# Optimization experiments

Measured on AMD Instinct MI355X. Metric: run time of the kernel, lower is better.

The kernel has to match this reference:

```python
import jax, jax.numpy as jnp
import numpy as np

N_NODES = 50000
N_EDGES = 800000
F_IN = 128
HID = 128
F_ADD = 32
N_GRAPHS = 128


def setup_inputs() -> dict:
    key = jax.random.key(0)
    ks = jax.random.split(key, 12)
    x = jax.random.normal(ks[0], (N_NODES, F_IN), dtype=jnp.float32)
    edge_index = jax.random.randint(ks[1], (2, N_EDGES), 0, N_NODES, dtype=jnp.int64)
    batch = jnp.sort(jax.random.randint(ks[2], (N_NODES,), 0, N_GRAPHS, dtype=jnp.int64))
    additional_features = jax.random.normal(ks[3], (N_GRAPHS, F_ADD), dtype=jnp.float32)
    def glorot(k, shape):
        fan_in, fan_out = shape[0], shape[1]
        lim = jnp.sqrt(6.0 / (fan_in + fan_out)).astype(jnp.float32)
        return jax.random.uniform(k, shape, jnp.float32, -lim, lim)
    W1 = glorot(ks[4], (F_IN, HID)); b1 = jnp.zeros((HID,), jnp.float32)
    W2 = glorot(ks[5], (HID, HID)); b2 = jnp.zeros((HID,), jnp.float32)
    fc1_w = glorot(ks[6], (HID + F_ADD, HID)); fc1_b = jnp.zeros((HID,), jnp.float32)
    fc2_w = glorot(ks[7], (HID, 2)); fc2_b = jnp.zeros((2,), jnp.float32)
    return {"x": x, "edge_index": edge_index, "batch": batch,
            "additional_features": additional_features,
            "W1": W1, "b1": b1, "W2": W2, "b2": b2,
            "fc1_w": fc1_w, "fc1_b": fc1_b, "fc2_w": fc2_w, "fc2_b": fc2_b}


def _gcn_conv(h, src, dst, norm, W, b):
    # h: [N, d_in]; symmetric-normalized scatter-add aggregation (PyG GCNConv)
    h = h @ W                                   # [N, d_out]
    msg = h[src] * norm[:, None]                # gather + scale: [E+N, d_out]
    return jax.ops.segment_sum(msg, dst, num_segments=N_NODES) + b


def reference(x, edge_index, batch, additional_features,
              W1, b1, W2, b2, fc1_w, fc1_b, fc2_w, fc2_b):
    loops = jnp.arange(N_NODES, dtype=edge_index.dtype)
    src = jnp.concatenate([edge_index[0], loops])   # A + I
    dst = jnp.concatenate([edge_index[1], loops])
    deg = jax.ops.segment_sum(jnp.ones_like(src, dtype=x.dtype), dst,
                              num_segments=N_NODES)
    dinv = jnp.where(deg > 0, jax.lax.rsqrt(jnp.maximum(deg, 1.0)), 0.0)
    norm = dinv[src] * dinv[dst]

    h = jax.nn.relu(_gcn_conv(x, src, dst, norm, W1, b1))
    h = jax.nn.relu(_gcn_conv(h, src, dst, norm, W2, b2))
    # dropout is identity in eval mode

    sums = jax.ops.segment_sum(h, batch, num_segments=N_GRAPHS)    # [G, HID]
    counts = jax.ops.segment_sum(jnp.ones((N_NODES,), h.dtype), batch,
                                 num_segments=N_GRAPHS)
    pooled = sums / jnp.maximum(counts, 1.0)[:, None]              # global_mean_pool

    z = jnp.concatenate([pooled, additional_features], axis=1)     # [G, HID+F_ADD]
    z = jax.nn.relu(z @ fc1_w + fc1_b)
    return z @ fc2_w + fc2_b                                       # [G, 2]
```

## Files before the change

kernel.cpp:

```cpp
#include <hip/hip_runtime.h>

#define NN 50000
#define NE 800000
#define FD 128
#define FDH 64
#define FA 32
#define NG 128
#define EETOT (NE + NN)
#define NBLK ((NN + 255) / 256)
#define PK 8
#define FEPB 2048
#define FNCH ((EETOT + FEPB - 1) / FEPB)
#define NPXCD 6250

typedef __attribute__((ext_vector_type(8))) short short8;
typedef __attribute__((ext_vector_type(4))) float f32x4;

__device__ __forceinline__ float bfbits(unsigned short u) {
    return __uint_as_float(((unsigned int)u) << 16);
}
__device__ __forceinline__ float bflo(unsigned int p) { return __uint_as_float(p << 16); }
__device__ __forceinline__ float bfhi(unsigned int p) { return __uint_as_float(p & 0xffff0000u); }
__device__ __forceinline__ unsigned short f2bf(float f) {
    unsigned int u = __float_as_uint(f);
    unsigned int r = u + 0x7FFFu + ((u >> 16) & 1u);
    return (unsigned short)(r >> 16);
}
__device__ __forceinline__ unsigned int packbf(float a, float b) {
    return (unsigned int)f2bf(a) | ((unsigned int)f2bf(b) << 16);
}
__device__ __forceinline__ int ld_idx(const int* p, int i, int is64) {
    return is64 ? p[2 * i] : p[i];
}
__device__ int probe_bf16(const unsigned int* t, int nwords) {
    int nz = 0, hits = 0;
    for (int i = 0; i < nwords; ++i) {
        unsigned int w = t[i];
        if (w == 0u) continue;
        ++nz;
        unsigned int e = (w >> 7) & 0xFFu;
        if (e >= 100u && e <= 140u) ++hits;
    }
    return (nz < 8) ? 1 : (hits * 4 >= nz * 3);
}

__global__ __launch_bounds__(128) void mark_kernel(float* out, float v) {
    out[threadIdx.x] = v;
}

__global__ __launch_bounds__(64) void flags_kernel(
        const unsigned int* x, const int* ei, const int* batch,
        const unsigned int* addf, const unsigned int* w1, const unsigned int* b1,
        const unsigned int* w2, const unsigned int* b2, const unsigned int* fc1w,
        const unsigned int* fc1b, const unsigned int* fc2w, const unsigned int* fc2b,
        int* flags) {
    if (threadIdx.x != 0) return;
    flags[0]  = probe_bf16(x, 64);
    flags[3]  = probe_bf16(addf, 64);
    flags[4]  = probe_bf16(w1, 64);
    flags[5]  = probe_bf16(b1, 64);
    flags[6]  = probe_bf16(w2, 64);
    flags[7]  = probe_bf16(b2, 64);
    flags[8]  = probe_bf16(fc1w, 64);
    flags[9]  = probe_bf16(fc1b, 64);
    flags[10] = probe_bf16(fc2w, 64);
    flags[11] = probe_bf16(fc2b, 1);
    int odd_or = 0;
    for (int k = 0; k < 32; ++k) odd_or |= ei[2 * k + 1];
    flags[12] = (odd_or == 0) ? 1 : 0;
    flags[13] = (batch[NN - 1] == 0) ? 1 : 0;
}

__global__ __launch_bounds__(256) void prep(
        const void* x, const void* addf,
        const void* w1, const void* b1, const void* w2, const void* b2,
        const void* fc1w, const void* fc1b, const void* fc2w, const void* fc2b,
        unsigned int* bufC, unsigned int* W1t, unsigned int* W2t,
        float* addff, float* b1f, float* b2f, float* fc1wf, float* fc1bf,
        float* fc2wf, float* fc2bf, const int* flags, int* degi) {
    int b = blockIdx.x;
    if (b < 12500) {
        int i = b * 256 + threadIdx.x;
        if (flags[0]) {
            bufC[i] = ((const unsigned int*)x)[i];
        } else {
            const float* s = (const float*)x;
            bufC[i] = packbf(s[2 * i], s[2 * i + 1]);
        }
    } else if (b < 12564) {
        int rel = (b - 12500) * 256 + threadIdx.x;
        const void* src = (rel < 8192) ? w1 : w2;
        unsigned int* dst = (rel < 8192) ? W1t : W2t;
        int flag = (rel < 8192) ? flags[4] : flags[6];
        int rr = rel & 8191;
        int n = rr >> 6, kk = rr & 63;
        float lo, hi;
        if (flag) {
            const unsigned short* s = (const unsigned short*)src;
            lo = bfbits(s[(2 * kk) * FD + n]);
            hi = bfbits(s[(2 * kk + 1) * FD + n]);
        } else {
            const float* s = (const float*)src;
            lo = s[(2 * kk) * FD + n];
            hi = s[(2 * kk + 1) * FD + n];
        }
        dst[rr] = packbf(lo, hi);
    } else if (b < 12663) {
        int i = (b - 12564) * 256 + threadIdx.x;
        const void* src; float* dst; int flag; int rel;
        if      (i < 4096)  { src = addf; dst = addff; flag = flags[3];  rel = i; }
        else if (i < 4224)  { src = b1;   dst = b1f;   flag = flags[5];  rel = i - 4096; }
        else if (i < 4352)  { src = b2;   dst = b2f;   flag = flags[7];  rel = i - 4224; }
        else if (i < 24832) { src = fc1w; dst = fc1wf; flag = flags[8];  rel = i - 4352; }
        else if (i < 24960) { src = fc1b; dst = fc1bf; flag = flags[9];  rel = i - 24832; }
        else if (i < 25216) { src = fc2w; dst = fc2wf; flag = flags[10]; rel = i - 24960; }
        else if (i < 25218) { src = fc2b; dst = fc2bf; flag = flags[11]; rel = i - 25216; }
        else return;
        if (flag) dst[rel] = bfbits(((const unsigned short*)src)[rel]);
        else      dst[rel] = ((const float*)src)[rel];
    } else {
        int i = (b - 12663) * 256 + threadIdx.x;
        if (i < NN) degi[i] = 0;
    }
}

__global__ __launch_bounds__(256) void deg_kernel(const int* ei, const int* flags,
                                                  int* deg) {
    int e = blockIdx.x * 256 + threadIdx.x;
    int is64 = flags[12];
    if (e < NE) atomicAdd(&deg[ld_idx(ei, NE + e, is64)], 1);
}

__global__ __launch_bounds__(256) void scan1(const int* deg, float* dinv,
                                             int* escan, int* bsum) {
    __shared__ int sh[256];
    int i = blockIdx.x * 256 + threadIdx.x;
    int d = (i < NN) ? deg[i] : 0;
    if (i < NN) dinv[i] = rsqrtf((float)(d + 1));
    int v = (i < NN) ? d + 1 : 0;
    sh[threadIdx.x] = v;
    __syncthreads();
    for (int off = 1; off < 256; off <<= 1) {
        int a = ((int)threadIdx.x >= off) ? sh[threadIdx.x - off] : 0;
        __syncthreads();
        sh[threadIdx.x] += a;
        __syncthreads();
    }
    if (i < NN) escan[i] = sh[threadIdx.x] - v;
    if (threadIdx.x == 255) bsum[blockIdx.x] = sh[255];
}

__global__ __launch_bounds__(256) void scan3(const int* escan, const int* bsum,
        const int* batch, const int* flags, int* rowstart, int* cursor, int* gstart) {
    __shared__ int sb[256];
    int t = threadIdx.x;
    int v = (t < NBLK) ? bsum[t] : 0;
    sb[t] = v;
    __syncthreads();
    for (int off = 1; off < 256; off <<= 1) {
        int a = (t >= off) ? sb[t - off] : 0;
        __syncthreads();
        sb[t] += a;
        __syncthreads();
    }
    int boff = (blockIdx.x == 0) ? 0 : sb[blockIdx.x - 1];
    int i = blockIdx.x * 256 + t;
    if (i < NN) {
        int r = escan[i] + boff;
        rowstart[i] = r;
        cursor[i]   = r;
    }
    if (i == 0) rowstart[NN] = EETOT;
    if (i < NN) {
        int is64 = flags[13];
        int bc = ld_idx(batch, i, is64);
        if (i == 0) {
            for (int g = 0; g <= bc; ++g) gstart[g] = 0;
        } else {
            int bp = ld_idx(batch, i - 1, is64);
            for (int g = bp + 1; g <= bc; ++g) gstart[g] = i;
        }
        if (i == NN - 1) {
            for (int g = bc + 1; g <= NG; ++g) gstart[g] = NN;
        }
    }
}

__global__ __launch_bounds__(256) void fill_kernel(const int* ei, const int* flags,
        const float* dinv, int* cursor, unsigned int* cv) {
    int chunk = blockIdx.x >> 3;
    int par   = blockIdx.x & 7;
    int base  = chunk * FEPB;
    int is64  = flags[12];
    #pragma unroll
    for (int k = 0; k < FEPB / 256; ++k) {
        int e = base + k * 256 + threadIdx.x;
        if (e >= EETOT) break;
        int s, d;
        if (e < NE) { d = ld_idx(ei, NE + e, is64); s = -1; }
        else        { s = d = e - NE; }
        if (d / NPXCD != par) continue;
        if (s < 0) s = ld_idx(ei, e, is64);
        int pos = atomicAdd(&cursor[d], 1);
        cv[pos] = (unsigned int)s | ((unsigned int)f2bf(dinv[s] * dinv[d]) << 16);
    }
}

__global__ __launch_bounds__(256) void gemm_mfma(const unsigned int* __restrict__ A,
        const unsigned int* __restrict__ Wt, unsigned short* __restrict__ C) {
    int wave = threadIdx.x >> 6;
    int lane = threadIdx.x & 63;
    int quad = lane >> 4;
    int l16  = lane & 15;
    int mbase = blockIdx.x * 64 + wave * 16;
    int ra = mbase + l16;
    if (ra >= NN) ra = NN - 1;
    short8 af[4];
    const uint4* Arow = (const uint4*)(A + (size_t)ra * FDH);
    #pragma unroll
    for (int kk = 0; kk < 4; ++kk) {
        uint4 v = Arow[kk * 4 + quad];
        af[kk] = *(short8*)&v;
    }
    #pragma unroll
    for (int nt = 0; nt < 8; ++nt) {
        int n = nt * 16 + l16;
        const uint4* Wrow = (const uint4*)(Wt + (size_t)n * FDH);
        f32x4 acc = {0.f, 0.f, 0.f, 0.f};
        #pragma unroll
        for (int kk = 0; kk < 4; ++kk) {
            uint4 wv = Wrow[kk * 4 + quad];
            short8 bf = *(short8*)&wv;
            acc = __builtin_amdgcn_mfma_f32_16x16x32_bf16(af[kk], bf, acc, 0, 0, 0);
        }
        int row0 = mbase + quad * 4;
        #pragma unroll
        for (int reg = 0; reg < 4; ++reg) {
            int r = row0 + reg;
            if (r < NN) C[(size_t)r * FD + nt * 16 + l16] = f2bf(acc[reg]);
        }
    }
}

__global__ __launch_bounds__(256) void aggregate_kernel(const unsigned int* Hb,
        const unsigned int* cv, const int* rowstart, const float* bias,
        unsigned int* outb) {
    int n = blockIdx.x * 4 + (threadIdx.x >> 6);
    int cp = threadIdx.x & 63;
    if (n >= NN) return;
    int jb = rowstart[n], je = rowstart[n + 1];
    float acc0 = 0.f, acc1 = 0.f;
    int j = jb;
    for (; j + 7 < je; j += 8) {
        unsigned int rr[8], hh[8];
        #pragma unroll
        for (int k = 0; k < 8; ++k) rr[k] = cv[j + k];
        #pragma unroll
        for (int k = 0; k < 8; ++k) hh[k] = Hb[(size_t)(rr[k] & 0xFFFFu) * FDH + cp];
        #pragma unroll
        for (int k = 0; k < 8; ++k) {
            float v = bfbits((unsigned short)(rr[k] >> 16));
            acc0 += v * bflo(hh[k]);
            acc1 += v * bfhi(hh[k]);
        }
    }
    for (; j + 3 < je; j += 4) {
        unsigned int rr[4], hh[4];
        #pragma unroll
        for (int k = 0; k < 4; ++k) rr[k] = cv[j + k];
        #pragma unroll
        for (int k = 0; k < 4; ++k) hh[k] = Hb[(size_t)(rr[k] & 0xFFFFu) * FDH + cp];
        #pragma unroll
        for (int k = 0; k < 4; ++k) {
            float v = bfbits((unsigned short)(rr[k] >> 16));
            acc0 += v * bflo(hh[k]);
            acc1 += v * bfhi(hh[k]);
        }
    }
    for (; j < je; ++j) {
        unsigned int r = cv[j];
        unsigned int h = Hb[(size_t)(r & 0xFFFFu) * FDH + cp];
        float v = bfbits((unsigned short)(r >> 16));
        acc0 += v * bflo(h);
        acc1 += v * bfhi(h);
    }
    acc0 = fmaxf(acc0 + bias[2 * cp], 0.f);
    acc1 = fmaxf(acc1 + bias[2 * cp + 1], 0.f);
    outb[(size_t)n * FDH + cp] = packbf(acc0, acc1);
}

__global__ __launch_bounds__(64) void pool_part(const unsigned int* Hb,
        const int* gstart, float* part) {
    int g = blockIdx.x >> 3;
    int k = blockIdx.x & (PK - 1);
    int cp = threadIdx.x;
    int s = gstart[g], e = gstart[g + 1];
    int len = e - s;
    int per = (len + PK - 1) / PK;
    int ss = s + k * per;
    int ee = ss + per; if (ee > e) ee = e;
    float a0 = 0.f, a1 = 0.f, b0 = 0.f, b1 = 0.f;
    int n = ss;
    for (; n + 1 < ee; n += 2) {
        unsigned int h0 = Hb[(size_t)n * FDH + cp];
        unsigned int h1 = Hb[(size_t)(n + 1) * FDH + cp];
        a0 += bflo(h0); a1 += bfhi(h0);
        b0 += bflo(h1); b1 += bfhi(h1);
    }
    if (n < ee) {
        unsigned int h0 = Hb[(size_t)n * FDH + cp];
        a0 += bflo(h0); a1 += bfhi(h0);
    }
    part[(size_t)(g * PK + k) * FD + 2 * cp]     = a0 + b0;
    part[(size_t)(g * PK + k) * FD + 2 * cp + 1] = a1 + b1;
}

__global__ __launch_bounds__(128) void head_kernel(const float* part, const int* gstart,
        const float* addf, const float* fc1w, const float* fc1b,
        const float* fc2w, const float* fc2b, const int* flags, void* outp) {
    int g = blockIdx.x;
    int t = threadIdx.x;
    __shared__ float z[FD + FA];
    __shared__ float h[FD];
    float a = 0.f;
    #pragma unroll
    for (int k = 0; k < PK; ++k) a += part[(size_t)(g * PK + k) * FD + t];
    float cnt = (float)(gstart[g + 1] - gstart[g]);
    if (cnt < 1.0f) cnt = 1.0f;
    z[t] = a / cnt;
    if (t < FA) z[FD + t] = addf[g * FA + t];
    __syncthreads();
    float acc = fc1b[t];
    #pragma unroll 4
    for (int k = 0; k < FD + FA; ++k)
        acc += z[k] * fc1w[k * FD + t];
    h[t] = fmaxf(acc, 0.f);
    __syncthreads();
    if (t < 2) {
        float o = fc2b[t];
        for (int j = 0; j < FD; ++j) o += h[j] * fc2w[j * 2 + t];
        if (flags[0]) ((unsigned short*)outp)[g * 2 + t] = f2bf(o);
        else          ((float*)outp)[g * 2 + t] = o;
    }
}

extern "C" void kernel_launch(void* const* d_in, const int* in_sizes, int n_in,
                              void* d_out, int out_size, void* d_ws, size_t ws_size,
                              hipStream_t stream) {
    (void)out_size;

    if (n_in != 12) {
        hipLaunchKernelGGL(mark_kernel, dim3(1), dim3(128), 0, stream,
                           (float*)d_out, 2000.0f);
        return;
    }
    const int exp_sizes[12] = {6400000, 1600000, 50000, 4096, 16384, 128,
                               16384, 128, 20480, 128, 256, 2};
    for (int i = 0; i < 12; ++i) {
        if (in_sizes[i] != exp_sizes[i]) {
            hipLaunchKernelGGL(mark_kernel, dim3(1), dim3(128), 0, stream,
                               (float*)d_out, 3000.0f + 100.0f * i);
            return;
        }
    }

    size_t off = 0;
    char* base = (char*)d_ws;
#define WSALLOC(ptr, type, nbytes) \
    type* ptr = (type*)(base + off); off += (((size_t)(nbytes)) + 255) & ~(size_t)255;
    WSALLOC(bufA,  unsigned int, (size_t)NN * FDH * 4)
    WSALLOC(bufB,  unsigned int, (size_t)NN * FDH * 4)
    WSALLOC(bufC,  unsigned int, (size_t)NN * FDH * 4)
    WSALLOC(dinv,  float, (size_t)NN * 4)
    WSALLOC(degi,  int,   (size_t)NN * 4)
    WSALLOC(rowst, int,   (size_t)(NN + 1) * 4)
    WSALLOC(cursor,int,   (size_t)NN * 4)
    WSALLOC(escan, int,   (size_t)NN * 4)
    WSALLOC(bsum,  int,   (size_t)NBLK * 4)
    WSALLOC(cv,    unsigned int, (size_t)EETOT * 4)
    WSALLOC(part,  float, (size_t)NG * PK * FD * 4)
    WSALLOC(gstart,int,   (size_t)(NG + 1) * 4)
    WSALLOC(W1t,   unsigned int, (size_t)FD * FDH * 4)
    WSALLOC(W2t,   unsigned int, (size_t)FD * FDH * 4)
    WSALLOC(b1f,   float, FD * 4)
    WSALLOC(b2f,   float, FD * 4)
    WSALLOC(addff, float, (size_t)NG * FA * 4)
    WSALLOC(fc1wf, float, (size_t)(FD + FA) * FD * 4)
    WSALLOC(fc1bf, float, FD * 4)
    WSALLOC(fc2wf, float, FD * 2 * 4)
    WSALLOC(fc2bf, float, 2 * 4)
    WSALLOC(flags, int, 16 * 4)
#undef WSALLOC
    if (ws_size < off) {
        hipLaunchKernelGGL(mark_kernel, dim3(1), dim3(128), 0, stream,
                           (float*)d_out, 1000.0f);
        return;
    }

    const int* ei    = (const int*)d_in[1];
    const int* batch = (const int*)d_in[2];

    hipLaunchKernelGGL(flags_kernel, dim3(1), dim3(64), 0, stream,
                       (const unsigned int*)d_in[0], ei, batch,
                       (const unsigned int*)d_in[3], (const unsigned int*)d_in[4],
                       (const unsigned int*)d_in[5], (const unsigned int*)d_in[6],
                       (const unsigned int*)d_in[7], (const unsigned int*)d_in[8],
                       (const unsigned int*)d_in[9], (const unsigned int*)d_in[10],
                       (const unsigned int*)d_in[11], flags);

    hipLaunchKernelGGL(prep, dim3(12859), dim3(256), 0, stream,
                       d_in[0], d_in[3], d_in[4], d_in[5], d_in[6],
                       d_in[7], d_in[8], d_in[9], d_in[10], d_in[11],
                       bufC, W1t, W2t, addff, b1f, b2f, fc1wf, fc1bf,
                       fc2wf, fc2bf, flags, degi);

    hipLaunchKernelGGL(deg_kernel, dim3((NE + 255) / 256), dim3(256), 0, stream,
                       ei, flags, degi);
    hipLaunchKernelGGL(scan1, dim3(NBLK), dim3(256), 0, stream,
                       degi, dinv, escan, bsum);
    hipLaunchKernelGGL(scan3, dim3(NBLK), dim3(256), 0, stream,
                       escan, bsum, batch, flags, rowst, cursor, gstart);
    hipLaunchKernelGGL(fill_kernel, dim3(FNCH * 8), dim3(256), 0, stream,
                       ei, flags, dinv, cursor, cv);

    hipLaunchKernelGGL(gemm_mfma, dim3((NN + 63) / 64), dim3(256), 0, stream,
                       bufC, W1t, (unsigned short*)bufA);
    hipLaunchKernelGGL(aggregate_kernel, dim3((NN + 3) / 4), dim3(256), 0, stream,
                       bufA, cv, rowst, b1f, bufB);
    hipLaunchKernelGGL(gemm_mfma, dim3((NN + 63) / 64), dim3(256), 0, stream,
                       bufB, W2t, (unsigned short*)bufA);
    hipLaunchKernelGGL(aggregate_kernel, dim3((NN + 3) / 4), dim3(256), 0, stream,
                       bufA, cv, rowst, b2f, bufB);

    hipLaunchKernelGGL(pool_part, dim3(NG * PK), dim3(64), 0, stream,
                       bufB, gstart, part);
    hipLaunchKernelGGL(head_kernel, dim3(NG), dim3(FD), 0, stream,
                       part, gstart, addff, fc1wf, fc1bf, fc2wf, fc2bf,
                       flags, d_out);
}
```

Before: 340.8 us.

## Fuse graph build into cooperative kernel, fold x conversion into GEMM, merge pool+head

Replaces the degree, scan, scan-finalize and CSR-fill kernels with one cooperative grid kernel that uses grid.sync between phases and caches 32-bit edge indices. The fp32-to-bf16 conversion of x moves into the first GEMM's load path, removing a separate full pass over x and the staging buffer. Pooling and the MLP head merge into one kernel, and the flag probes use wave ballots instead of a serial loop. This cuts launch count and memory traffic but adds grid-wide barrier costs and extra s32/d32 buffers, and reduces pooling parallelism to one block per graph.

```diff
diff --git a/kernel.cpp b/kernel.cpp
--- a/kernel.cpp
+++ b/kernel.cpp
@@ -1,4 +1,7 @@
 #include <hip/hip_runtime.h>
+#include <hip/hip_cooperative_groups.h>
+
+namespace cg = cooperative_groups;
 
 #define NN 50000
 #define NE 800000
@@ -8,10 +11,11 @@
 #define NG 128
 #define EETOT (NE + NN)
 #define NBLK ((NN + 255) / 256)
-#define PK 8
 #define FEPB 2048
 #define FNCH ((EETOT + FEPB - 1) / FEPB)
 #define NPXCD 6250
+#define CBG 1024
+#define CBT (CBG * 256)
 
 typedef __attribute__((ext_vector_type(8))) short short8;
 typedef __attribute__((ext_vector_type(4))) float f32x4;
@@ -32,63 +36,48 @@
 __device__ __forceinline__ int ld_idx(const int* p, int i, int is64) {
     return is64 ? p[2 * i] : p[i];
 }
-__device__ int probe_bf16(const unsigned int* t, int nwords) {
-    int nz = 0, hits = 0;
-    for (int i = 0; i < nwords; ++i) {
-        unsigned int w = t[i];
-        if (w == 0u) continue;
-        ++nz;
-        unsigned int e = (w >> 7) & 0xFFu;
-        if (e >= 100u && e <= 140u) ++hits;
-    }
-    return (nz < 8) ? 1 : (hits * 4 >= nz * 3);
-}
 
 __global__ __launch_bounds__(128) void mark_kernel(float* out, float v) {
     out[threadIdx.x] = v;
 }
 
-__global__ __launch_bounds__(64) void flags_kernel(
+__global__ __launch_bounds__(256) void flags_kernel(
         const unsigned int* x, const int* ei, const int* batch,
         const unsigned int* addf, const unsigned int* w1, const unsigned int* b1,
         const unsigned int* w2, const unsigned int* b2, const unsigned int* fc1w,
         const unsigned int* fc1b, const unsigned int* fc2w, const unsigned int* fc2b,
         int* flags) {
-    if (threadIdx.x != 0) return;
-    flags[0]  = probe_bf16(x, 64);
-    flags[3]  = probe_bf16(addf, 64);
-    flags[4]  = probe_bf16(w1, 64);
-    flags[5]  = probe_bf16(b1, 64);
-    flags[6]  = probe_bf16(w2, 64);
-    flags[7]  = probe_bf16(b2, 64);
-    flags[8]  = probe_bf16(fc1w, 64);
-    flags[9]  = probe_bf16(fc1b, 64);
-    flags[10] = probe_bf16(fc2w, 64);
-    flags[11] = probe_bf16(fc2b, 1);
-    int odd_or = 0;
-    for (int k = 0; k < 32; ++k) odd_or |= ei[2 * k + 1];
-    flags[12] = (odd_or == 0) ? 1 : 0;
-    flags[13] = (batch[NN - 1] == 0) ? 1 : 0;
+    int w = threadIdx.x >> 6, lane = threadIdx.x & 63;
+    const unsigned int* tp[12] = {x, 0, 0, addf, w1, b1, w2, b2, fc1w, fc1b, fc2w, fc2b};
+    const int nw[12] = {64, 0, 0, 64, 64, 64, 64, 64, 64, 64, 64, 1};
+    for (int idx = w; idx < 12; idx += 4) {
+        const unsigned int* p = tp[idx];
+        if (!p) continue;
+        unsigned int wv = (lane < nw[idx]) ? p[lane] : 0u;
+        int nzp = (wv != 0u) ? 1 : 0;
+        unsigned int e = (wv >> 7) & 0xFFu;
+        int hitp = (nzp && e >= 100u && e <= 140u) ? 1 : 0;
+        int nz = __popcll(__ballot(nzp));
+        int hits = __popcll(__ballot(hitp));
+        if (lane == 0) flags[idx] = (nz < 8) ? 1 : (hits * 4 >= nz * 3);
+    }
+    if (w == 1) {
+        int v = (lane < 32) ? ei[2 * lane + 1] : 0;
+        unsigned long long m = __ballot(v != 0);
+        if (lane == 0) flags[12] = (m == 0ull) ? 1 : 0;
+    }
+    if (w == 2 && lane == 0) flags[13] = (batch[NN - 1] == 0) ? 1 : 0;
 }
 
 __global__ __launch_bounds__(256) void prep(
-        const void* x, const void* addf,
-        const void* w1, const void* b1, const void* w2, const void* b2,
-        const void* fc1w, const void* fc1b, const void* fc2w, const void* fc2b,
-        unsigned int* bufC, unsigned int* W1t, unsigned int* W2t,
+        const void* addf, const void* w1, const void* b1, const void* w2,
+        const void* b2, const void* fc1w, const void* fc1b, const void* fc2w,
+        const void* fc2b, unsigned int* W1t, unsigned int* W2t,
         float* addff, float* b1f, float* b2f, float* fc1wf, float* fc1bf,
         float* fc2wf, float* fc2bf, const int* flags, int* degi) {
     int b = blockIdx.x;
-    if (b < 12500) {
-        int i = b * 256 + threadIdx.x;
-        if (flags[0]) {
-            bufC[i] = ((const unsigned int*)x)[i];
-        } else {
-            const float* s = (const float*)x;
-            bufC[i] = packbf(s[2 * i], s[2 * i + 1]);
-        }
-    } else if (b < 12564) {
-        int rel = (b - 12500) * 256 + threadIdx.x;
+    if (b < 64) {
+        int rel = b * 256 + threadIdx.x;
         const void* src = (rel < 8192) ? w1 : w2;
         unsigned int* dst = (rel < 8192) ? W1t : W2t;
         int flag = (rel < 8192) ? flags[4] : flags[6];
@@ -105,8 +94,8 @@
             hi = s[(2 * kk + 1) * FD + n];
         }
         dst[rr] = packbf(lo, hi);
-    } else if (b < 12663) {
-        int i = (b - 12564) * 256 + threadIdx.x;
+    } else if (b < 163) {
+        int i = (b - 64) * 256 + threadIdx.x;
         const void* src; float* dst; int flag; int rel;
         if      (i < 4096)  { src = addf; dst = addff; flag = flags[3];  rel = i; }
         else if (i < 4224)  { src = b1;   dst = b1f;   flag = flags[5];  rel = i - 4096; }
@@ -119,8 +108,104 @@
         if (flag) dst[rel] = bfbits(((const unsigned short*)src)[rel]);
         else      dst[rel] = ((const float*)src)[rel];
     } else {
-        int i = (b - 12663) * 256 + threadIdx.x;
+        int i = (b - 163) * 256 + threadIdx.x;
         if (i < NN) degi[i] = 0;
+    }
+}
+
+__global__ __launch_bounds__(256, 4) void coop_build(
+        const int* ei, const int* batch, const int* flags,
+        int* degi, float* dinv, int* escan, int* bsum,
+        int* rowstart, int* cursor, int* gstart,
+        int* s32, int* d32, unsigned int* cv) {
+    cg::grid_group grid = cg::this_grid();
+    __shared__ int sh[256];
+    int tid = blockIdx.x * 256 + threadIdx.x;
+    int b = blockIdx.x;
+    int is64 = flags[12];
+
+    for (int e = tid; e < NE; e += CBT) {
+        int s = ld_idx(ei, e, is64);
+        int d = ld_idx(ei, NE + e, is64);
+        s32[e] = s;
+        d32[e] = d;
+        atomicAdd(&degi[d], 1);
+    }
+    grid.sync();
+
+    if (b < NBLK) {
+        int i = b * 256 + threadIdx.x;
+        int d = (i < NN) ? degi[i] : 0;
+        if (i < NN) dinv[i] = rsqrtf((float)(d + 1));
+        int v = (i < NN) ? d + 1 : 0;
+        sh[threadIdx.x] = v;
+        __syncthreads();
+        for (int off = 1; off < 256; off <<= 1) {
+            int a = ((int)threadIdx.x >= off) ? sh[threadIdx.x - off] : 0;
+            __syncthreads();
+            sh[threadIdx.x] += a;
+            __syncthreads();
+        }
+        if (i < NN) escan[i] = sh[threadIdx.x] - v;
+        if (threadIdx.x == 255) bsum[b] = sh[255];
+    }
+    grid.sync();
+
+    if (b == 0) {
+        int t = threadIdx.x;
+        int v = (t < NBLK) ? bsum[t] : 0;
+        sh[t] = v;
+        __syncthreads();
+        for (int off = 1; off < 256; off <<= 1) {
+            int a = (t >= off) ? sh[t - off] : 0;
+            __syncthreads();
+            sh[t] += a;
+            __syncthreads();
+        }
+        if (t < NBLK) bsum[t] = sh[t] - v;
+    }
+    grid.sync();
+
+    if (b < NBLK) {
+        int i = b * 256 + threadIdx.x;
+        if (i < NN) {
+            int r = escan[i] + bsum[b];
+            rowstart[i] = r;
+            cursor[i]   = r;
+        }
+        if (i == 0) rowstart[NN] = EETOT;
+        if (i < NN) {
+            int is64b = flags[13];
+            int bc = ld_idx(batch, i, is64b);
+            if (i == 0) {
+                for (int g = 0; g <= bc; ++g) gstart[g] = 0;
+            } else {
+                int bp = ld_idx(batch, i - 1, is64b);
+                for (int g = bp + 1; g <= bc; ++g) gstart[g] = i;
+            }
+            if (i == NN - 1) {
+                for (int g = bc + 1; g <= NG; ++g) gstart[g] = NN;
+            }
+        }
+    }
+    grid.sync();
+
+    for (int vb = b; vb < FNCH * 8; vb += CBG) {
+        int chunk = vb >> 3;
+        int par   = vb & 7;
+        int base  = chunk * FEPB;
+        #pragma unroll
+        for (int k = 0; k < FEPB / 256; ++k) {
+            int e = base + k * 256 + threadIdx.x;
+            if (e >= EETOT) break;
+            int s, d;
+            if (e < NE) { d = d32[e]; s = -1; }
+            else        { s = d = e - NE; }
+            if (d / NPXCD != par) continue;
+            if (s < 0) s = s32[e];
+            int pos = atomicAdd(&cursor[d], 1);
+            cv[pos] = (unsigned int)s | ((unsigned int)f2bf(dinv[s] * dinv[d]) << 16);
+        }
     }
 }
 
@@ -206,8 +291,9 @@
     }
 }
 
-__global__ __launch_bounds__(256) void gemm_mfma(const unsigned int* __restrict__ A,
-        const unsigned int* __restrict__ Wt, unsigned short* __restrict__ C) {
+__global__ __launch_bounds__(256) void gemm_mfma(const void* __restrict__ Av,
+        const unsigned int* __restrict__ Wt, unsigned short* __restrict__ C,
+        const int* flags, int maybe_f32) {
     int wave = threadIdx.x >> 6;
     int lane = threadIdx.x & 63;
     int quad = lane >> 4;
@@ -216,11 +302,25 @@
     int ra = mbase + l16;
     if (ra >= NN) ra = NN - 1;
     short8 af[4];
-    const uint4* Arow = (const uint4*)(A + (size_t)ra * FDH);
-    #pragma unroll
-    for (int kk = 0; kk < 4; ++kk) {
-        uint4 v = Arow[kk * 4 + quad];
-        af[kk] = *(short8*)&v;
+    bool f32in = maybe_f32 && !flags[0];
+    if (!f32in) {
+        const uint4* Arow = (const uint4*)((const unsigned int*)Av + (size_t)ra * FDH);
+        #pragma unroll
+        for (int kk = 0; kk < 4; ++kk) {
+            uint4 v = Arow[kk * 4 + quad];
+            af[kk] = *(short8*)&v;
+        }
+    } else {
+        const float* Arow = (const float*)Av + (size_t)ra * FD;
+        #pragma unroll
+        for (int kk = 0; kk < 4; ++kk) {
+            const float4* p = (const float4*)(Arow + (kk * 4 + quad) * 8);
+            float4 u = p[0], v = p[1];
+            uint4 q;
+            q.x = packbf(u.x, u.y); q.y = packbf(u.z, u.w);
+            q.z = packbf(v.x, v.y); q.w = packbf(v.z, v.w);
+            af[kk] = *(short8*)&q;
+        }
     }
     #pragma unroll
     for (int nt = 0; nt < 8; ++nt) {
@@ -289,52 +389,40 @@
     outb[(size_t)n * FDH + cp] = packbf(acc0, acc1);
 }
 
-__global__ __launch_bounds__(64) void pool_part(const unsigned int* Hb,
-        const int* gstart, float* part) {
-    int g = blockIdx.x >> 3;
-    int k = blockIdx.x & (PK - 1);
-    int cp = threadIdx.x;
-    int s = gstart[g], e = gstart[g + 1];
-    int len = e - s;
-    int per = (len + PK - 1) / PK;
-    int ss = s + k * per;
-    int ee = ss + per; if (ee > e) ee = e;
-    float a0 = 0.f, a1 = 0.f, b0 = 0.f, b1 = 0.f;
-    int n = ss;
-    for (; n + 1 < ee; n += 2) {
-        unsigned int h0 = Hb[(size_t)n * FDH + cp];
-        unsigned int h1 = Hb[(size_t)(n + 1) * FDH + cp];
-        a0 += bflo(h0); a1 += bfhi(h0);
-        b0 += bflo(h1); b1 += bfhi(h1);
-    }
-    if (n < ee) {
-        unsigned int h0 = Hb[(size_t)n * FDH + cp];
-        a0 += bflo(h0); a1 += bfhi(h0);
-    }
-    part[(size_t)(g * PK + k) * FD + 2 * cp]     = a0 + b0;
-    part[(size_t)(g * PK + k) * FD + 2 * cp + 1] = a1 + b1;
-}
-
-__global__ __launch_bounds__(128) void head_kernel(const float* part, const int* gstart,
-        const float* addf, const float* fc1w, const float* fc1b,
+__global__ __launch_bounds__(256) void poolhead(const unsigned int* Hb,
+        const int* gstart, const float* addf, const float* fc1w, const float* fc1b,
         const float* fc2w, const float* fc2b, const int* flags, void* outp) {
     int g = blockIdx.x;
     int t = threadIdx.x;
+    int q = t >> 6, w = t & 63;
+    int s = gstart[g], e = gstart[g + 1];
+    float a0 = 0.f, a1 = 0.f;
+    #pragma unroll 4
+    for (int n = s + q; n < e; n += 4) {
+        unsigned int h = Hb[(size_t)n * FDH + w];
+        a0 += bflo(h);
+        a1 += bfhi(h);
+    }
+    __shared__ float pp[4][FD];
     __shared__ float z[FD + FA];
     __shared__ float h[FD];
-    float a = 0.f;
-    #pragma unroll
-    for (int k = 0; k < PK; ++k) a += part[(size_t)(g * PK + k) * FD + t];
-    float cnt = (float)(gstart[g + 1] - gstart[g]);
-    if (cnt < 1.0f) cnt = 1.0f;
-    z[t] = a / cnt;
-    if (t < FA) z[FD + t] = addf[g * FA + t];
+    pp[q][2 * w]     = a0;
+    pp[q][2 * w + 1] = a1;
     __syncthreads();
-    float acc = fc1b[t];
-    #pragma unroll 4
-    for (int k = 0; k < FD + FA; ++k)
-        acc += z[k] * fc1w[k * FD + t];
-    h[t] = fmaxf(acc, 0.f);
+    if (t < FD) {
+        float cnt = (float)(e - s);
+        if (cnt < 1.0f) cnt = 1.0f;
+        z[t] = (pp[0][t] + pp[1][t] + pp[2][t] + pp[3][t]) / cnt;
+    }
+    if (t >= FD && t < FD + FA) z[t] = addf[g * FA + (t - FD)];
+    __syncthreads();
+    if (t < FD) {
+        float acc = fc1b[t];
+        #pragma unroll 4
+        for (int k = 0; k < FD + FA; ++k)
+            acc += z[k] * fc1w[k * FD + t];
+        h[t] = fmaxf(acc, 0.f);
+    }
     __syncthreads();
     if (t < 2) {
         float o = fc2b[t];
@@ -370,7 +458,6 @@
     type* ptr = (type*)(base + off); off += (((size_t)(nbytes)) + 255) & ~(size_t)255;
     WSALLOC(bufA,  unsigned int, (size_t)NN * FDH * 4)
     WSALLOC(bufB,  unsigned int, (size_t)NN * FDH * 4)
-    WSALLOC(bufC,  unsigned int, (size_t)NN * FDH * 4)
     WSALLOC(dinv,  float, (size_t)NN * 4)
     WSALLOC(degi,  int,   (size_t)NN * 4)
     WSALLOC(rowst, int,   (size_t)(NN + 1) * 4)
@@ -378,8 +465,9 @@
     WSALLOC(escan, int,   (size_t)NN * 4)
     WSALLOC(bsum,  int,   (size_t)NBLK * 4)
     WSALLOC(cv,    unsigned int, (size_t)EETOT * 4)
-    WSALLOC(part,  float, (size_t)NG * PK * FD * 4)
     WSALLOC(gstart,int,   (size_t)(NG + 1) * 4)
+    WSALLOC(s32,   int,   (size_t)NE * 4)
+    WSALLOC(d32,   int,   (size_t)NE * 4)
     WSALLOC(W1t,   unsigned int, (size_t)FD * FDH * 4)
     WSALLOC(W2t,   unsigned int, (size_t)FD * FDH * 4)
     WSALLOC(b1f,   float, FD * 4)
@@ -400,7 +488,7 @@
     const int* ei    = (const int*)d_in[1];
     const int* batch = (const int*)d_in[2];
 
-    hipLaunchKernelGGL(flags_kernel, dim3(1), dim3(64), 0, stream,
+    hipLaunchKernelGGL(flags_kernel, dim3(1), dim3(256), 0, stream,
                        (const unsigned int*)d_in[0], ei, batch,
                        (const unsigned int*)d_in[3], (const unsigned int*)d_in[4],
                        (const unsigned int*)d_in[5], (const unsigned int*)d_in[6],
@@ -408,33 +496,47 @@
                        (const unsigned int*)d_in[9], (const unsigned int*)d_in[10],
                        (const unsigned int*)d_in[11], flags);
 
-    hipLaunchKernelGGL(prep, dim3(12859), dim3(256), 0, stream,
-                       d_in[0], d_in[3], d_in[4], d_in[5], d_in[6],
-                       d_in[7], d_in[8], d_in[9], d_in[10], d_in[11],
-                       bufC, W1t, W2t, addff, b1f, b2f, fc1wf, fc1bf,
+    hipLaunchKernelGGL(prep, dim3(359), dim3(256), 0, stream,
+                       d_in[3], d_in[4], d_in[5], d_in[6], d_in[7],
+                       d_in[8], d_in[9], d_in[10], d_in[11],
+                       W1t, W2t, addff, b1f, b2f, fc1wf, fc1bf,
                        fc2wf, fc2bf, flags, degi);
 
-    hipLaunchKernelGGL(deg_kernel, dim3((NE + 255) / 256), dim3(256), 0, stream,
-                       ei, flags, degi);
-    hipLaunchKernelGGL(scan1, dim3(NBLK), dim3(256), 0, stream,
-                       degi, dinv, escan, bsum);
-    hipLaunchKernelGGL(scan3, dim3(NBLK), dim3(256), 0, stream,
-                       escan, bsum, batch, flags, rowst, cursor, gstart);
-    hipLaunchKernelGGL(fill_kernel, dim3(FNCH * 8), dim3(256), 0, stream,
-                       ei, flags, dinv, cursor, cv);
+    {
+        const int* eiA = ei;
+        const int* batchA = batch;
+        const int* flagsA = flags;
+        void* cbArgs[13] = {
+            (void*)&eiA, (void*)&batchA, (void*)&flagsA,
+            (void*)&degi, (void*)&dinv, (void*)&escan, (void*)&bsum,
+            (void*)&rowst, (void*)&cursor, (void*)&gstart,
+            (void*)&s32, (void*)&d32, (void*)&cv
+        };
+        hipError_t cerr = hipLaunchCooperativeKernel(
+            reinterpret_cast<void*>(coop_build), dim3(CBG), dim3(256),
+            cbArgs, 0, stream);
+        if (cerr != hipSuccess) {
+            hipLaunchKernelGGL(deg_kernel, dim3((NE + 255) / 256), dim3(256), 0,
+                               stream, ei, flags, degi);
+            hipLaunchKernelGGL(scan1, dim3(NBLK), dim3(256), 0, stream,
+                               degi, dinv, escan, bsum);
+            hipLaunchKernelGGL(scan3, dim3(NBLK), dim3(256), 0, stream,
+                               escan, bsum, batch, flags, rowst, cursor, gstart);
+            hipLaunchKernelGGL(fill_kernel, dim3(FNCH * 8), dim3(256), 0, stream,
+                               ei, flags, dinv, cursor, cv);
+        }
+    }
 
     hipLaunchKernelGGL(gemm_mfma, dim3((NN + 63) / 64), dim3(256), 0, stream,
-                       bufC, W1t, (unsigned short*)bufA);
+                       d_in[0], W1t, (unsigned short*)bufA, flags, 1);
     hipLaunchKernelGGL(aggregate_kernel, dim3((NN + 3) / 4), dim3(256), 0, stream,
                        bufA, cv, rowst, b1f, bufB);
     hipLaunchKernelGGL(gemm_mfma, dim3((NN + 63) / 64), dim3(256), 0, stream,
-                       bufB, W2t, (unsigned short*)bufA);
+                       bufB, W2t, (unsigned short*)bufA, flags, 0);
     hipLaunchKernelGGL(aggregate_kernel, dim3((NN + 3) / 4), dim3(256), 0, stream,
                        bufA, cv, rowst, b2f, bufB);
 
-    hipLaunchKernelGGL(pool_part, dim3(NG * PK), dim3(64), 0, stream,
-                       bufB, gstart, part);
-    hipLaunchKernelGGL(head_kernel, dim3(NG), dim3(FD), 0, stream,
-                       part, gstart, addff, fc1wf, fc1bf, fc2wf, fc2bf,
+    hipLaunchKernelGGL(poolhead, dim3(NG), dim3(256), 0, stream,
+                       bufB, gstart, addff, fc1wf, fc1bf, fc2wf, fc2bf,
                        flags, d_out);
 }
```

Result: slower. 764.8 us (+124.4%).
